# Performance work log

Hardware: AMD Instinct MI355X
Metric: run time of the kernel (lower is better)

## Reference

```python
import jax, jax.numpy as jnp
import numpy as np

B, P, D = 8, 1024, 768
H = 12
HD = D // H


def setup_inputs() -> dict:
    key = jax.random.key(0)
    k1, k2, k3, k4, k5 = jax.random.split(key, 5)
    s = 0.02
    return {
        "x": jax.random.normal(k1, (B, P, D), dtype=jnp.float32),
        "w_qkv": jax.random.normal(k2, (D, 3 * D), dtype=jnp.float32) * s,
        "b_qkv": jax.random.normal(k3, (3 * D,), dtype=jnp.float32) * s,
        "w_proj": jax.random.normal(k4, (D, D), dtype=jnp.float32) * s,
        "b_proj": jax.random.normal(k5, (D,), dtype=jnp.float32) * s,
    }


def reference(x, w_qkv, b_qkv, w_proj, b_proj):
    b, p, d = x.shape
    scale = HD ** -0.5
    qkv = x @ w_qkv + b_qkv                      # [B,P,3D]
    qkv = qkv.reshape(b, p, 3, H, HD).transpose(2, 0, 3, 1, 4)  # [3,B,H,P,HD]
    q, k, v = qkv[0], qkv[1], qkv[2]
    attn = jnp.einsum("bhqd,bhkd->bhqk", q, k) * scale
    attn = jax.nn.softmax(attn, axis=-1)         # attn_drop is identity (p=0)
    weighted_avg = jnp.einsum("bhqk,bhkd->bhqd", attn, v)
    weighted_avg = weighted_avg.transpose(0, 2, 1, 3).reshape(b, p, d)  # [B,P,D]
    out = weighted_avg @ w_proj + b_proj         # proj_drop is identity (p=0)
    return (out, weighted_avg)
```

## Files before the change

### kernel.cpp

```cpp
#include <hip/hip_runtime.h>
#include <hip/hip_bf16.h>


typedef __attribute__((ext_vector_type(8))) short short8;
typedef __attribute__((ext_vector_type(4))) float f32x4;

#define MFMA_BF16(a, b, c) __builtin_amdgcn_mfma_f32_16x16x32_bf16((a), (b), (c), 0, 0, 0)

#define NB 8
#define NP 1024
#define ND 768
#define NH 12
#define NHD 64
#define NTOK (NB * NP)
#define N3D (3 * ND)
#define OUT_HALF (NTOK * ND)
#define QSCALE 0.18033688f

__device__ __forceinline__ void gload_lds16(const void* gptr, void* ldsptr) {
  __builtin_amdgcn_global_load_lds(
      (const __attribute__((address_space(1))) unsigned int*)gptr,
      (__attribute__((address_space(3))) unsigned int*)ldsptr, 16, 0, 0);
}

__device__ __forceinline__ unsigned pack_bf16x2(float a, float b) {
  __hip_bfloat162 h = __float22bfloat162_rn(float2{a, b});
  return *reinterpret_cast<unsigned*>(&h);
}

__device__ __forceinline__ int swz_g(int b) { return b ^ (((b >> 7) & 7) << 4); }


__global__ void k_cvt_x(const float* __restrict__ in, __hip_bfloat16* __restrict__ out) {
  int i = (blockIdx.x * 256 + threadIdx.x) * 8;
  float4 a = *(const float4*)(in + i);
  float4 b = *(const float4*)(in + i + 4);
  union { __hip_bfloat16 h[8]; uint4 u; } r;
  r.h[0] = __float2bfloat16(a.x); r.h[1] = __float2bfloat16(a.y);
  r.h[2] = __float2bfloat16(a.z); r.h[3] = __float2bfloat16(a.w);
  r.h[4] = __float2bfloat16(b.x); r.h[5] = __float2bfloat16(b.y);
  r.h[6] = __float2bfloat16(b.z); r.h[7] = __float2bfloat16(b.w);
  *(uint4*)(out + i) = r.u;
}

__global__ void k_cvt_t(const float* __restrict__ in, __hip_bfloat16* __restrict__ out,
                        int K, int N) {
  __shared__ float tile[32][33];
  int k0 = blockIdx.x * 32;
  int n0 = blockIdx.y * 32;
  int r = threadIdx.x >> 5;
  int c = threadIdx.x & 31;
#pragma unroll
  for (int i = 0; i < 4; ++i)
    tile[r + 8 * i][c] = in[(size_t)(k0 + r + 8 * i) * N + n0 + c];
  __syncthreads();
#pragma unroll
  for (int i = 0; i < 4; ++i)
    out[(size_t)(n0 + r + 8 * i) * K + k0 + c] = __float2bfloat16(tile[c][r + 8 * i]);
}


__device__ __forceinline__ void gemm_mainloop(const __hip_bfloat16* __restrict__ A,
                                              const __hip_bfloat16* __restrict__ BT,
                                              int m0, int n0, char* Ls,
                                              f32x4 acc[4][4]) {
  const int tid = threadIdx.x;
  const int wid = tid >> 6, lane = tid & 63;
  const int wm = wid >> 1, wn = wid & 1;
  const int lrow = lane & 15, lk = lane >> 4;
  constexpr int K = 768, NKT = K / 64;

  int aoff[4][2], boff[4][2];
#pragma unroll
  for (int i = 0; i < 4; ++i)
#pragma unroll
    for (int kh = 0; kh < 2; ++kh) {
      aoff[i][kh] = swz_g((wm * 64 + i * 16 + lrow) * 128 + kh * 64 + lk * 16);
      boff[i][kh] = swz_g((wn * 64 + i * 16 + lrow) * 128 + kh * 64 + lk * 16);
    }

#define STAGE_G(kt, bi)                                                  \
  {                                                                      \
    const int k0s = (kt) * 64;                                           \
    char* dst = Ls + (bi) * 32768;                                       \
    _Pragma("unroll")                                                    \
    for (int t = 0; t < 4; ++t) {                                        \
      const int L = t * 4096 + tid * 16;           \
      const int lb = swz_g(L);                         \
      const int mr = lb >> 7;                  \
      const int kk = (lb & 127) >> 1;           \
      gload_lds16(A + (size_t)(m0 + mr) * K + k0s + kk, dst + L);        \
      gload_lds16(BT + (size_t)(n0 + mr) * K + k0s + kk,                 \
                  dst + 16384 + L);                                      \
    }                                                                    \
  }

  STAGE_G(0, 0);
  STAGE_G(1, 1);

#pragma unroll 2
  for (int kt = 0; kt < NKT - 1; ++kt) {
    asm volatile("s_waitcnt vmcnt(8)" ::: "memory");
    __builtin_amdgcn_s_barrier();

    const char* buf = Ls + (kt & 1) * 32768;
    short8 af[4][2], bf[4][2];
#pragma unroll
    for (int i = 0; i < 4; ++i)
#pragma unroll
      for (int kh = 0; kh < 2; ++kh) {
        af[i][kh] = *(const short8*)(buf + aoff[i][kh]);
        bf[i][kh] = *(const short8*)(buf + 16384 + boff[i][kh]);
      }

    asm volatile("s_waitcnt lgkmcnt(0)" ::: "memory");
    __builtin_amdgcn_s_barrier();

    if (kt + 2 < NKT) STAGE_G(kt + 2, kt & 1);

#pragma unroll
    for (int kh = 0; kh < 2; ++kh)
#pragma unroll
      for (int mi = 0; mi < 4; ++mi)
#pragma unroll
        for (int ni = 0; ni < 4; ++ni)
          acc[mi][ni] = MFMA_BF16(af[mi][kh], bf[ni][kh], acc[mi][ni]);
  }

  asm volatile("s_waitcnt vmcnt(0)" ::: "memory");
  __builtin_amdgcn_s_barrier();
  {
    const char* buf = Ls + ((NKT - 1) & 1) * 32768;
    short8 af[4][2], bf[4][2];
#pragma unroll
    for (int i = 0; i < 4; ++i)
#pragma unroll
      for (int kh = 0; kh < 2; ++kh) {
        af[i][kh] = *(const short8*)(buf + aoff[i][kh]);
        bf[i][kh] = *(const short8*)(buf + 16384 + boff[i][kh]);
      }
#pragma unroll
    for (int kh = 0; kh < 2; ++kh)
#pragma unroll
      for (int mi = 0; mi < 4; ++mi)
#pragma unroll
        for (int ni = 0; ni < 4; ++ni)
          acc[mi][ni] = MFMA_BF16(af[mi][kh], bf[ni][kh], acc[mi][ni]);
  }
#undef STAGE_G
}


__launch_bounds__(256)
__global__ void k_qkv_gemm(const __hip_bfloat16* __restrict__ A,
                           const __hip_bfloat16* __restrict__ BT,
                           const float* __restrict__ bias,
                           __hip_bfloat16* __restrict__ q_ws,
                           __hip_bfloat16* __restrict__ k_ws,
                           __hip_bfloat16* __restrict__ v_ws) {
  __shared__ char Ls[2 * 32768];
  const int mt = blockIdx.x & 63, nt = blockIdx.x >> 6;
  const int m0 = mt * 128, n0 = nt * 128;
  const int wid = threadIdx.x >> 6, lane = threadIdx.x & 63;
  const int wm = wid >> 1, wn = wid & 1;
  const int lrow = lane & 15, lk = lane >> 4;

  f32x4 acc[4][4] = {};
  gemm_mainloop(A, BT, m0, n0, Ls, acc);

  const int which = n0 / ND;
#pragma unroll
  for (int ni = 0; ni < 4; ++ni) {
    const int n = n0 + wn * 64 + ni * 16 + lrow;
    const float bv = bias[n];
    const int hh = (n % ND) >> 6;
    const int hd = n & 63;
#pragma unroll
    for (int mi = 0; mi < 4; ++mi) {
      const int mbase = m0 + wm * 64 + mi * 16 + lk * 4;
#pragma unroll
      for (int i = 0; i < 4; ++i) {
        const int m = mbase + i;
        const float v = acc[mi][ni][i] + bv;
        const int b = m >> 10, p = m & 1023;
        const int bh = b * NH + hh;
        if (which == 0)      q_ws[((size_t)bh * NP + p) * NHD + hd] = __float2bfloat16(v * QSCALE);
        else if (which == 1) k_ws[((size_t)bh * NP + p) * NHD + hd] = __float2bfloat16(v);
        else                 v_ws[((size_t)bh * NHD + hd) * NP + p] = __float2bfloat16(v);
      }
    }
  }
}


#define KVBLK 64

__launch_bounds__(256)
__global__ void k_attn(const __hip_bfloat16* __restrict__ q_ws,
                       const __hip_bfloat16* __restrict__ k_ws,
                       const __hip_bfloat16* __restrict__ v_ws,
                       float* __restrict__ wavg_f32,
                       __hip_bfloat16* __restrict__ wavg_bf) {
  __shared__ char smem[2 * 16384 + 4 * 4608];
  const int bid = blockIdx.x;
  const int wg = (bid & 7) * 96 + (bid >> 3);
  const int bh = wg >> 3, qb = wg & 7;
  const int tid = threadIdx.x;
  const int wid = tid >> 6, lane = tid & 63;
  const int lrow = lane & 15, lk = lane >> 4;
  const int q0 = qb * 128 + wid * 32;
  char* pbuf = smem + 32768 + wid * 4608;

  const __hip_bfloat16* Qb = q_ws + (size_t)bh * NP * NHD;
  const __hip_bfloat16* Kb = k_ws + (size_t)bh * NP * NHD;
  const __hip_bfloat16* Vb = v_ws + (size_t)bh * NHD * NP;

  short8 qf[2][2];
#pragma unroll
  for (int g = 0; g < 2; ++g) {
    qf[g][0] = *(const short8*)(Qb + (size_t)(q0 + g * 16 + lrow) * NHD + lk * 8);
    qf[g][1] = *(const short8*)(Qb + (size_t)(q0 + g * 16 + lrow) * NHD + 32 + lk * 8);
  }

  f32x4 acc[2][4] = {};
  float dsum[2] = {0.f, 0.f};

#define STAGE(buf, key0)                                                          \
  {                                                                               \
    _Pragma("unroll")                                                             \
    for (int p = 0; p < 2; ++p) {                                                 \
      const int L = p * 4096 + tid * 16;                                          \
      const int r = L >> 7;                                                       \
      const int cb = L & 127;                                                     \
      const int sc = (cb ^ ((r & 7) << 4)) >> 1;        \
      gload_lds16(Kb + (size_t)((key0) + r) * NHD + sc, (buf) + L);               \
      gload_lds16(Vb + (size_t)r * NP + (key0) + sc, (buf) + 8192 + L);           \
    }                                                                             \
  }

  char* cur = smem;
  char* nxt = smem + 16384;
  STAGE(cur, 0);
  __syncthreads();

  for (int kc = 0; kc < NP / KVBLK; ++kc) {
    if (kc < NP / KVBLK - 1) STAGE(nxt, (kc + 1) * KVBLK);

    char* Ks = cur;
    char* Vs = cur + 8192;

    f32x4 s[2][4];
    __builtin_amdgcn_s_setprio(1);
#pragma unroll
    for (int kt = 0; kt < 4; ++kt) {
      const int row = kt * 16 + lrow;
      const int sw = (row & 7) << 4;
      short8 klo = *(const short8*)(Ks + row * 128 + ((lk * 16) ^ sw));
      short8 khi = *(const short8*)(Ks + row * 128 + ((64 + lk * 16) ^ sw));
      f32x4 z = {0.f, 0.f, 0.f, 0.f};
      s[0][kt] = MFMA_BF16(klo, qf[0][0], z);
      s[0][kt] = MFMA_BF16(khi, qf[0][1], s[0][kt]);
      s[1][kt] = MFMA_BF16(klo, qf[1][0], z);
      s[1][kt] = MFMA_BF16(khi, qf[1][1], s[1][kt]);
    }
    __builtin_amdgcn_s_setprio(0);

#pragma unroll
    for (int g = 0; g < 2; ++g)
#pragma unroll
      for (int kt = 0; kt < 4; ++kt) {
        const float p0 = __builtin_amdgcn_exp2f(s[g][kt][0]);
        const float p1 = __builtin_amdgcn_exp2f(s[g][kt][1]);
        const float p2 = __builtin_amdgcn_exp2f(s[g][kt][2]);
        const float p3 = __builtin_amdgcn_exp2f(s[g][kt][3]);
        dsum[g] += (p0 + p1) + (p2 + p3);
        uint2 w;
        w.x = pack_bf16x2(p0, p1);
        w.y = pack_bf16x2(p2, p3);
        *(uint2*)(pbuf + (g * 16 + lrow) * 144 + kt * 32 + lk * 8) = w;
      }

    __builtin_amdgcn_s_setprio(1);
#pragma unroll
    for (int kh = 0; kh < 2; ++kh) {
      short8 a20 = *(const short8*)(pbuf + lrow * 144 + kh * 64 + lk * 16);
      short8 a21 = *(const short8*)(pbuf + (16 + lrow) * 144 + kh * 64 + lk * 16);
#pragma unroll
      for (int hdt = 0; hdt < 4; ++hdt) {
        const int row = hdt * 16 + lrow;
        short8 vf = *(const short8*)(Vs + row * 128 +
                                     ((kh * 64 + lk * 16) ^ ((row & 7) << 4)));
        acc[0][hdt] = MFMA_BF16(a20, vf, acc[0][hdt]);
        acc[1][hdt] = MFMA_BF16(a21, vf, acc[1][hdt]);
      }
    }
    __builtin_amdgcn_s_setprio(0);

    __syncthreads();
    char* t = cur; cur = nxt; nxt = t;
  }

  const int b = bh / NH, hh = bh % NH;
#pragma unroll
  for (int g = 0; g < 2; ++g) {
    float ds = dsum[g];
    ds += __shfl_xor(ds, 16);
    ds += __shfl_xor(ds, 32);
    float rd[4];
#pragma unroll
    for (int i = 0; i < 4; ++i) rd[i] = 1.0f / __shfl(ds, lk * 4 + i, 16);

#pragma unroll
    for (int hdt = 0; hdt < 4; ++hdt) {
#pragma unroll
      for (int i = 0; i < 4; ++i) {
        const int qq = q0 + g * 16 + lk * 4 + i;
        const int col = hh * NHD + hdt * 16 + lrow;
        const float val = acc[g][hdt][i] * rd[i];
        const size_t o = ((size_t)b * NP + qq) * ND + col;
        wavg_f32[o] = val;
        wavg_bf[o] = __float2bfloat16(val);
      }
    }
  }
#undef STAGE
}


__launch_bounds__(256)
__global__ void k_proj_gemm(const __hip_bfloat16* __restrict__ A,
                            const __hip_bfloat16* __restrict__ BT,
                            const float* __restrict__ bias,
                            float* __restrict__ C) {
  __shared__ char Ls[2 * 32768];
  const int mt = blockIdx.x & 63, nt = blockIdx.x >> 6;
  const int m0 = mt * 128, n0 = nt * 128;
  const int wid = threadIdx.x >> 6, lane = threadIdx.x & 63;
  const int wm = wid >> 1, wn = wid & 1;
  const int lrow = lane & 15, lk = lane >> 4;

  f32x4 acc[4][4] = {};
  gemm_mainloop(A, BT, m0, n0, Ls, acc);

#pragma unroll
  for (int ni = 0; ni < 4; ++ni) {
    const int n = n0 + wn * 64 + ni * 16 + lrow;
    const float bv = bias[n];
#pragma unroll
    for (int mi = 0; mi < 4; ++mi) {
      const int mbase = m0 + wm * 64 + mi * 16 + lk * 4;
#pragma unroll
      for (int i = 0; i < 4; ++i)
        C[(size_t)(mbase + i) * ND + n] = acc[mi][ni][i] + bv;
    }
  }
}


extern "C" void kernel_launch(void* const* d_in, const int* in_sizes, int n_in,
                              void* d_out, int out_size, void* d_ws, size_t ws_size,
                              hipStream_t stream) {
  const float* x      = (const float*)d_in[0];
  const float* w_qkv  = (const float*)d_in[1];
  const float* b_qkv  = (const float*)d_in[2];
  const float* w_proj = (const float*)d_in[3];
  const float* b_proj = (const float*)d_in[4];
  float* out = (float*)d_out;
  float* wavg_out = out + OUT_HALF;

  char* ws = (char*)d_ws;
  __hip_bfloat16* xbf    = (__hip_bfloat16*)(ws);
  __hip_bfloat16* wqkvT  = (__hip_bfloat16*)(ws + 12582912);
  __hip_bfloat16* wprojT = (__hip_bfloat16*)(ws + 16121856);
  __hip_bfloat16* q_ws   = (__hip_bfloat16*)(ws + 17301504);
  __hip_bfloat16* k_ws   = (__hip_bfloat16*)(ws + 29884416);
  __hip_bfloat16* v_ws   = (__hip_bfloat16*)(ws + 42467328);
  __hip_bfloat16* wavg_bf = xbf;

  k_cvt_x<<<NTOK * ND / (256 * 8), 256, 0, stream>>>(x, xbf);
  k_cvt_t<<<dim3(ND / 32, N3D / 32), 256, 0, stream>>>(w_qkv, wqkvT, ND, N3D);
  k_cvt_t<<<dim3(ND / 32, ND / 32), 256, 0, stream>>>(w_proj, wprojT, ND, ND);
  k_qkv_gemm<<<(NTOK / 128) * (N3D / 128), 256, 0, stream>>>(xbf, wqkvT, b_qkv,
                                                             q_ws, k_ws, v_ws);
  k_attn<<<(NP / 128) * (NB * NH), 256, 0, stream>>>(q_ws, k_ws, v_ws, wavg_out, wavg_bf);
  k_proj_gemm<<<(NTOK / 128) * (ND / 128), 256, 0, stream>>>(wavg_bf, wprojT, b_proj, out);
}
```

Before: 131.0 us.

## Enlarge QKV GEMM tile to 256x256 with 512 threads and split-K staging

Rewrites the QKV projection GEMM to use 256x256 output tiles computed by 8 waves (each 128x64). The K=64 step is staged in two 32-wide halves, so each half can be refilled right after it is consumed. Blocks are remapped for L2 locality, and MFMA sections raise wave priority. The larger tile cuts global and LDS traffic per FLOP, but it uses 128KB of LDS and more accumulator registers per thread, and launches only 288 blocks, which may hurt occupancy and tail balance on the GPU.

```diff
diff --git a/kernel.cpp b/kernel.cpp
--- a/kernel.cpp
+++ b/kernel.cpp
@@ -60,6 +60,109 @@
 }
 
 
+__launch_bounds__(512, 2)
+__global__ void k_qkv_gemm(const __hip_bfloat16* __restrict__ A,
+                           const __hip_bfloat16* __restrict__ BT,
+                           const float* __restrict__ bias,
+                           __hip_bfloat16* __restrict__ q_ws,
+                           __hip_bfloat16* __restrict__ k_ws,
+                           __hip_bfloat16* __restrict__ v_ws) {
+  __shared__ char Ls[2 * 65536];
+  constexpr int K = 768, NKT = K / 64;
+  const int bid = blockIdx.x;
+  const int wg = (bid & 7) * 36 + (bid >> 3);
+  const int mt = wg & 31, nt = wg >> 5;
+  const int m0 = mt * 256, n0 = nt * 256;
+  const int tid = threadIdx.x;
+  const int wid = tid >> 6, lane = tid & 63;
+  const int wm = wid >> 2, wn = wid & 3;
+  const int lrow = lane & 15, lk = lane >> 4;
+
+  int aoff[8], boff[4];
+#pragma unroll
+  for (int i = 0; i < 8; ++i)
+    aoff[i] = swz_g((wm * 128 + i * 16 + lrow) * 64 + lk * 16);
+#pragma unroll
+  for (int j = 0; j < 4; ++j)
+    boff[j] = swz_g((wn * 64 + j * 16 + lrow) * 64 + lk * 16);
+
+#define QSTAGE(kt, kh)                                                      \
+  {                                                                         \
+    const int k0s = (kt) * 64 + (kh) * 32;                                  \
+    char* bufb = Ls + ((kt) & 1) * 65536;                                   \
+    _Pragma("unroll")                                                       \
+    for (int t = 0; t < 2; ++t) {                                           \
+      const int L = t * 8192 + tid * 16;     \
+      const int lb = swz_g(L);                                              \
+      const int mr = lb >> 6;                     \
+      const int kk = (lb & 63) >> 1;               \
+      gload_lds16(A + (size_t)(m0 + mr) * K + k0s + kk,                     \
+                  bufb + (kh) * 16384 + L);                                 \
+      gload_lds16(BT + (size_t)(n0 + mr) * K + k0s + kk,                    \
+                  bufb + 32768 + (kh) * 16384 + L);                         \
+    }                                                                       \
+  }
+
+  QSTAGE(0, 0); QSTAGE(0, 1); QSTAGE(1, 0); QSTAGE(1, 1);
+
+  f32x4 acc[8][4] = {};
+
+#pragma unroll 2
+  for (int kt = 0; kt < NKT; ++kt) {
+    if (kt < NKT - 1) asm volatile("s_waitcnt vmcnt(8)" ::: "memory");
+    else              asm volatile("s_waitcnt vmcnt(0)" ::: "memory");
+    __builtin_amdgcn_s_barrier();
+
+    const char* bufb = Ls + (kt & 1) * 65536;
+#pragma unroll
+    for (int kh = 0; kh < 2; ++kh) {
+      const char* Ac = bufb + kh * 16384;
+      const char* Bc = bufb + 32768 + kh * 16384;
+      short8 af[8], bf[4];
+#pragma unroll
+      for (int j = 0; j < 4; ++j) bf[j] = *(const short8*)(Bc + boff[j]);
+#pragma unroll
+      for (int i = 0; i < 8; ++i) af[i] = *(const short8*)(Ac + aoff[i]);
+
+      __builtin_amdgcn_s_setprio(1);
+#pragma unroll
+      for (int i = 0; i < 8; ++i)
+#pragma unroll
+        for (int j = 0; j < 4; ++j)
+          acc[i][j] = MFMA_BF16(af[i], bf[j], acc[i][j]);
+      __builtin_amdgcn_s_setprio(0);
+
+      __builtin_amdgcn_s_barrier();
+      if (kt + 2 < NKT) QSTAGE(kt + 2, kh);
+    }
+  }
+#undef QSTAGE
+
+  const int which = n0 / ND;
+#pragma unroll
+  for (int j = 0; j < 4; ++j) {
+    const int n = n0 + wn * 64 + j * 16 + lrow;
+    const float bv = bias[n];
+    const int hh = (n % ND) >> 6;
+    const int hd = n & 63;
+#pragma unroll
+    for (int i = 0; i < 8; ++i) {
+      const int mbase = m0 + wm * 128 + i * 16 + lk * 4;
+#pragma unroll
+      for (int r = 0; r < 4; ++r) {
+        const int m = mbase + r;
+        const float v = acc[i][j][r] + bv;
+        const int b = m >> 10, p = m & 1023;
+        const int bh = b * NH + hh;
+        if (which == 0)      q_ws[((size_t)bh * NP + p) * NHD + hd] = __float2bfloat16(v * QSCALE);
+        else if (which == 1) k_ws[((size_t)bh * NP + p) * NHD + hd] = __float2bfloat16(v);
+        else                 v_ws[((size_t)bh * NHD + hd) * NP + p] = __float2bfloat16(v);
+      }
+    }
+  }
+}
+
+
 __device__ __forceinline__ void gemm_mainloop(const __hip_bfloat16* __restrict__ A,
                                               const __hip_bfloat16* __restrict__ BT,
                                               int m0, int n0, char* Ls,
@@ -85,10 +188,10 @@
     char* dst = Ls + (bi) * 32768;                                       \
     _Pragma("unroll")                                                    \
     for (int t = 0; t < 4; ++t) {                                        \
-      const int L = t * 4096 + tid * 16;           \
-      const int lb = swz_g(L);                         \
-      const int mr = lb >> 7;                  \
-      const int kk = (lb & 127) >> 1;           \
+      const int L = t * 4096 + tid * 16;                                 \
+      const int lb = swz_g(L);                                           \
+      const int mr = lb >> 7;                                            \
+      const int kk = (lb & 127) >> 1;                                    \
       gload_lds16(A + (size_t)(m0 + mr) * K + k0s + kk, dst + L);        \
       gload_lds16(BT + (size_t)(n0 + mr) * K + k0s + kk,                 \
                   dst + 16384 + L);                                      \
@@ -148,48 +251,6 @@
           acc[mi][ni] = MFMA_BF16(af[mi][kh], bf[ni][kh], acc[mi][ni]);
   }
 #undef STAGE_G
-}
-
-
-__launch_bounds__(256)
-__global__ void k_qkv_gemm(const __hip_bfloat16* __restrict__ A,
-                           const __hip_bfloat16* __restrict__ BT,
-                           const float* __restrict__ bias,
-                           __hip_bfloat16* __restrict__ q_ws,
-                           __hip_bfloat16* __restrict__ k_ws,
-                           __hip_bfloat16* __restrict__ v_ws) {
-  __shared__ char Ls[2 * 32768];
-  const int mt = blockIdx.x & 63, nt = blockIdx.x >> 6;
-  const int m0 = mt * 128, n0 = nt * 128;
-  const int wid = threadIdx.x >> 6, lane = threadIdx.x & 63;
-  const int wm = wid >> 1, wn = wid & 1;
-  const int lrow = lane & 15, lk = lane >> 4;
-
-  f32x4 acc[4][4] = {};
-  gemm_mainloop(A, BT, m0, n0, Ls, acc);
-
-  const int which = n0 / ND;
-#pragma unroll
-  for (int ni = 0; ni < 4; ++ni) {
-    const int n = n0 + wn * 64 + ni * 16 + lrow;
-    const float bv = bias[n];
-    const int hh = (n % ND) >> 6;
-    const int hd = n & 63;
-#pragma unroll
-    for (int mi = 0; mi < 4; ++mi) {
-      const int mbase = m0 + wm * 64 + mi * 16 + lk * 4;
-#pragma unroll
-      for (int i = 0; i < 4; ++i) {
-        const int m = mbase + i;
-        const float v = acc[mi][ni][i] + bv;
-        const int b = m >> 10, p = m & 1023;
-        const int bh = b * NH + hh;
-        if (which == 0)      q_ws[((size_t)bh * NP + p) * NHD + hd] = __float2bfloat16(v * QSCALE);
-        else if (which == 1) k_ws[((size_t)bh * NP + p) * NHD + hd] = __float2bfloat16(v);
-        else                 v_ws[((size_t)bh * NHD + hd) * NP + p] = __float2bfloat16(v);
-      }
-    }
-  }
 }
 
 
@@ -232,7 +293,7 @@
       const int L = p * 4096 + tid * 16;                                          \
       const int r = L >> 7;                                                       \
       const int cb = L & 127;                                                     \
-      const int sc = (cb ^ ((r & 7) << 4)) >> 1;        \
+      const int sc = (cb ^ ((r & 7) << 4)) >> 1;                                  \
       gload_lds16(Kb + (size_t)((key0) + r) * NHD + sc, (buf) + L);               \
       gload_lds16(Vb + (size_t)r * NP + (key0) + sc, (buf) + 8192 + L);           \
     }                                                                             \
@@ -380,7 +441,7 @@
   k_cvt_x<<<NTOK * ND / (256 * 8), 256, 0, stream>>>(x, xbf);
   k_cvt_t<<<dim3(ND / 32, N3D / 32), 256, 0, stream>>>(w_qkv, wqkvT, ND, N3D);
   k_cvt_t<<<dim3(ND / 32, ND / 32), 256, 0, stream>>>(w_proj, wprojT, ND, ND);
-  k_qkv_gemm<<<(NTOK / 128) * (N3D / 128), 256, 0, stream>>>(xbf, wqkvT, b_qkv,
+  k_qkv_gemm<<<(NTOK / 256) * (N3D / 256), 512, 0, stream>>>(xbf, wqkvT, b_qkv,
                                                              q_ws, k_ws, v_ws);
   k_attn<<<(NP / 128) * (NB * NH), 256, 0, stream>>>(q_ws, k_ws, v_ws, wavg_out, wavg_bf);
   k_proj_gemm<<<(NTOK / 128) * (ND / 128), 256, 0, stream>>>(wavg_bf, wprojT, b_proj, out);
```

Measured after the change: 178.1 us. 1.36x slower.

## Use two waves of 64 query rows each in attention kernel

Applied to the files above, without the earlier changes.

The attention block drops from four waves to two, and each wave now handles 64 query rows instead of 32. This doubles reuse of each K/V fragment loaded from LDS across MFMAs. Score computation and exp are also interleaved per key tile so softmax work overlaps with MFMA issue. In exchange, register pressure rises (acc grows to 4x4), each block has fewer waves to hide latency, and staging needs more load instructions per thread.

```diff
diff --git a/kernel.cpp b/kernel.cpp
--- a/kernel.cpp
+++ b/kernel.cpp
@@ -195,41 +195,41 @@
 
 #define KVBLK 64
 
-__launch_bounds__(256)
+__launch_bounds__(128)
 __global__ void k_attn(const __hip_bfloat16* __restrict__ q_ws,
                        const __hip_bfloat16* __restrict__ k_ws,
                        const __hip_bfloat16* __restrict__ v_ws,
                        float* __restrict__ wavg_f32,
                        __hip_bfloat16* __restrict__ wavg_bf) {
-  __shared__ char smem[2 * 16384 + 4 * 4608];
+  __shared__ char smem[2 * 16384 + 2 * 9216];
   const int bid = blockIdx.x;
   const int wg = (bid & 7) * 96 + (bid >> 3);
   const int bh = wg >> 3, qb = wg & 7;
   const int tid = threadIdx.x;
   const int wid = tid >> 6, lane = tid & 63;
   const int lrow = lane & 15, lk = lane >> 4;
-  const int q0 = qb * 128 + wid * 32;
-  char* pbuf = smem + 32768 + wid * 4608;
+  const int q0 = qb * 128 + wid * 64;
+  char* pbuf = smem + 32768 + wid * 9216;
 
   const __hip_bfloat16* Qb = q_ws + (size_t)bh * NP * NHD;
   const __hip_bfloat16* Kb = k_ws + (size_t)bh * NP * NHD;
   const __hip_bfloat16* Vb = v_ws + (size_t)bh * NHD * NP;
 
-  short8 qf[2][2];
-#pragma unroll
-  for (int g = 0; g < 2; ++g) {
+  short8 qf[4][2];
+#pragma unroll
+  for (int g = 0; g < 4; ++g) {
     qf[g][0] = *(const short8*)(Qb + (size_t)(q0 + g * 16 + lrow) * NHD + lk * 8);
     qf[g][1] = *(const short8*)(Qb + (size_t)(q0 + g * 16 + lrow) * NHD + 32 + lk * 8);
   }
 
-  f32x4 acc[2][4] = {};
-  float dsum[2] = {0.f, 0.f};
+  f32x4 acc[4][4] = {};
+  float dsum[4] = {0.f, 0.f, 0.f, 0.f};
 
 #define STAGE(buf, key0)                                                          \
   {                                                                               \
     _Pragma("unroll")                                                             \
-    for (int p = 0; p < 2; ++p) {                                                 \
-      const int L = p * 4096 + tid * 16;                                          \
+    for (int p = 0; p < 4; ++p) {                                                 \
+      const int L = p * 2048 + tid * 16;                                          \
       const int r = L >> 7;                                                       \
       const int cb = L & 127;                                                     \
       const int sc = (cb ^ ((r & 7) << 4)) >> 1;        \
@@ -249,52 +249,53 @@
     char* Ks = cur;
     char* Vs = cur + 8192;
 
-    f32x4 s[2][4];
-    __builtin_amdgcn_s_setprio(1);
 #pragma unroll
     for (int kt = 0; kt < 4; ++kt) {
       const int row = kt * 16 + lrow;
       const int sw = (row & 7) << 4;
       short8 klo = *(const short8*)(Ks + row * 128 + ((lk * 16) ^ sw));
       short8 khi = *(const short8*)(Ks + row * 128 + ((64 + lk * 16) ^ sw));
-      f32x4 z = {0.f, 0.f, 0.f, 0.f};
-      s[0][kt] = MFMA_BF16(klo, qf[0][0], z);
-      s[0][kt] = MFMA_BF16(khi, qf[0][1], s[0][kt]);
-      s[1][kt] = MFMA_BF16(klo, qf[1][0], z);
-      s[1][kt] = MFMA_BF16(khi, qf[1][1], s[1][kt]);
-    }
-    __builtin_amdgcn_s_setprio(0);
-
-#pragma unroll
-    for (int g = 0; g < 2; ++g)
-#pragma unroll
-      for (int kt = 0; kt < 4; ++kt) {
-        const float p0 = __builtin_amdgcn_exp2f(s[g][kt][0]);
-        const float p1 = __builtin_amdgcn_exp2f(s[g][kt][1]);
-        const float p2 = __builtin_amdgcn_exp2f(s[g][kt][2]);
-        const float p3 = __builtin_amdgcn_exp2f(s[g][kt][3]);
+      f32x4 s[4];
+      __builtin_amdgcn_s_setprio(1);
+#pragma unroll
+      for (int g = 0; g < 4; ++g) {
+        f32x4 z = {0.f, 0.f, 0.f, 0.f};
+        s[g] = MFMA_BF16(klo, qf[g][0], z);
+        s[g] = MFMA_BF16(khi, qf[g][1], s[g]);
+      }
+      __builtin_amdgcn_s_setprio(0);
+#pragma unroll
+      for (int g = 0; g < 4; ++g) {
+        const float p0 = __builtin_amdgcn_exp2f(s[g][0]);
+        const float p1 = __builtin_amdgcn_exp2f(s[g][1]);
+        const float p2 = __builtin_amdgcn_exp2f(s[g][2]);
+        const float p3 = __builtin_amdgcn_exp2f(s[g][3]);
         dsum[g] += (p0 + p1) + (p2 + p3);
         uint2 w;
         w.x = pack_bf16x2(p0, p1);
         w.y = pack_bf16x2(p2, p3);
         *(uint2*)(pbuf + (g * 16 + lrow) * 144 + kt * 32 + lk * 8) = w;
       }
-
-    __builtin_amdgcn_s_setprio(1);
+    }
+
 #pragma unroll
     for (int kh = 0; kh < 2; ++kh) {
-      short8 a20 = *(const short8*)(pbuf + lrow * 144 + kh * 64 + lk * 16);
-      short8 a21 = *(const short8*)(pbuf + (16 + lrow) * 144 + kh * 64 + lk * 16);
+      short8 a2[4];
+#pragma unroll
+      for (int g = 0; g < 4; ++g)
+        a2[g] = *(const short8*)(pbuf + (g * 16 + lrow) * 144 + kh * 64 + lk * 16);
+      __builtin_amdgcn_s_setprio(1);
 #pragma unroll
       for (int hdt = 0; hdt < 4; ++hdt) {
         const int row = hdt * 16 + lrow;
         short8 vf = *(const short8*)(Vs + row * 128 +
                                      ((kh * 64 + lk * 16) ^ ((row & 7) << 4)));
-        acc[0][hdt] = MFMA_BF16(a20, vf, acc[0][hdt]);
-        acc[1][hdt] = MFMA_BF16(a21, vf, acc[1][hdt]);
-      }
-    }
-    __builtin_amdgcn_s_setprio(0);
+#pragma unroll
+        for (int g = 0; g < 4; ++g)
+          acc[g][hdt] = MFMA_BF16(a2[g], vf, acc[g][hdt]);
+      }
+      __builtin_amdgcn_s_setprio(0);
+    }
 
     __syncthreads();
     char* t = cur; cur = nxt; nxt = t;
@@ -302,7 +303,7 @@
 
   const int b = bh / NH, hh = bh % NH;
 #pragma unroll
-  for (int g = 0; g < 2; ++g) {
+  for (int g = 0; g < 4; ++g) {
     float ds = dsum[g];
     ds += __shfl_xor(ds, 16);
     ds += __shfl_xor(ds, 32);
@@ -382,6 +383,6 @@
   k_cvt_t<<<dim3(ND / 32, ND / 32), 256, 0, stream>>>(w_proj, wprojT, ND, ND);
   k_qkv_gemm<<<(NTOK / 128) * (N3D / 128), 256, 0, stream>>>(xbf, wqkvT, b_qkv,
                                                              q_ws, k_ws, v_ws);
-  k_attn<<<(NP / 128) * (NB * NH), 256, 0, stream>>>(q_ws, k_ws, v_ws, wavg_out, wavg_bf);
+  k_attn<<<(NP / 128) * (NB * NH), 128, 0, stream>>>(q_ws, k_ws, v_ws, wavg_out, wavg_bf);
   k_proj_gemm<<<(NTOK / 128) * (ND / 128), 256, 0, stream>>>(wavg_bf, wprojT, b_proj, out);
 }
```

New measurement: 132.7 us. About the same (+1.3%).

## Load K/V fragments directly from global memory instead of LDS double-buffering

Applied to the files above, without the earlier changes.

Drops the double-buffered global-to-LDS staging of K and V tiles and the per-iteration block barrier in the attention kernel. Each wave now reads its K and V MFMA fragments straight from global memory, relying on L1/L2 caches for reuse across the four waves. This cuts LDS use, which may allow higher occupancy, and removes synchronisation. The cost is that each wave re-reads K/V from global memory with higher latency and no explicit prefetch overlap.

```diff
diff --git a/kernel.cpp b/kernel.cpp
--- a/kernel.cpp
+++ b/kernel.cpp
@@ -201,7 +201,7 @@
                        const __hip_bfloat16* __restrict__ v_ws,
                        float* __restrict__ wavg_f32,
                        __hip_bfloat16* __restrict__ wavg_bf) {
-  __shared__ char smem[2 * 16384 + 4 * 4608];
+  __shared__ char pbuf_all[4 * 4608];
   const int bid = blockIdx.x;
   const int wg = (bid & 7) * 96 + (bid >> 3);
   const int bh = wg >> 3, qb = wg & 7;
@@ -209,7 +209,7 @@
   const int wid = tid >> 6, lane = tid & 63;
   const int lrow = lane & 15, lk = lane >> 4;
   const int q0 = qb * 128 + wid * 32;
-  char* pbuf = smem + 32768 + wid * 4608;
+  char* pbuf = pbuf_all + wid * 4608;
 
   const __hip_bfloat16* Qb = q_ws + (size_t)bh * NP * NHD;
   const __hip_bfloat16* Kb = k_ws + (size_t)bh * NP * NHD;
@@ -225,38 +225,16 @@
   f32x4 acc[2][4] = {};
   float dsum[2] = {0.f, 0.f};
 
-#define STAGE(buf, key0)                                                          \
-  {                                                                               \
-    _Pragma("unroll")                                                             \
-    for (int p = 0; p < 2; ++p) {                                                 \
-      const int L = p * 4096 + tid * 16;                                          \
-      const int r = L >> 7;                                                       \
-      const int cb = L & 127;                                                     \
-      const int sc = (cb ^ ((r & 7) << 4)) >> 1;        \
-      gload_lds16(Kb + (size_t)((key0) + r) * NHD + sc, (buf) + L);               \
-      gload_lds16(Vb + (size_t)r * NP + (key0) + sc, (buf) + 8192 + L);           \
-    }                                                                             \
-  }
-
-  char* cur = smem;
-  char* nxt = smem + 16384;
-  STAGE(cur, 0);
-  __syncthreads();
-
   for (int kc = 0; kc < NP / KVBLK; ++kc) {
-    if (kc < NP / KVBLK - 1) STAGE(nxt, (kc + 1) * KVBLK);
-
-    char* Ks = cur;
-    char* Vs = cur + 8192;
+    const int key0 = kc * KVBLK;
 
     f32x4 s[2][4];
     __builtin_amdgcn_s_setprio(1);
 #pragma unroll
     for (int kt = 0; kt < 4; ++kt) {
-      const int row = kt * 16 + lrow;
-      const int sw = (row & 7) << 4;
-      short8 klo = *(const short8*)(Ks + row * 128 + ((lk * 16) ^ sw));
-      short8 khi = *(const short8*)(Ks + row * 128 + ((64 + lk * 16) ^ sw));
+      const int row = key0 + kt * 16 + lrow;
+      short8 klo = *(const short8*)(Kb + (size_t)row * NHD + lk * 8);
+      short8 khi = *(const short8*)(Kb + (size_t)row * NHD + 32 + lk * 8);
       f32x4 z = {0.f, 0.f, 0.f, 0.f};
       s[0][kt] = MFMA_BF16(klo, qf[0][0], z);
       s[0][kt] = MFMA_BF16(khi, qf[0][1], s[0][kt]);
@@ -287,17 +265,13 @@
       short8 a21 = *(const short8*)(pbuf + (16 + lrow) * 144 + kh * 64 + lk * 16);
 #pragma unroll
       for (int hdt = 0; hdt < 4; ++hdt) {
-        const int row = hdt * 16 + lrow;
-        short8 vf = *(const short8*)(Vs + row * 128 +
-                                     ((kh * 64 + lk * 16) ^ ((row & 7) << 4)));
+        short8 vf = *(const short8*)(Vb + (size_t)(hdt * 16 + lrow) * NP +
+                                     key0 + kh * 32 + lk * 8);
         acc[0][hdt] = MFMA_BF16(a20, vf, acc[0][hdt]);
         acc[1][hdt] = MFMA_BF16(a21, vf, acc[1][hdt]);
       }
     }
     __builtin_amdgcn_s_setprio(0);
-
-    __syncthreads();
-    char* t = cur; cur = nxt; nxt = t;
   }
 
   const int b = bh / NH, hh = bh % NH;
@@ -323,7 +297,6 @@
       }
     }
   }
-#undef STAGE
 }
 
 
```

Measured after the change: 174.5 us. 33.2% more time.
